# Kernel optimization log

Hardware: AMD Instinct MI355X
Metric: run time of the kernel (lower is better)

The kernel has to match this reference:

```python
import jax, jax.numpy as jnp
import numpy as np
from functools import partial

B, C, H, W = 64, 3, 64, 64
D = 64            # hidden_dim == slot dim
S = 7             # num_slots
ITERS = 3
EPS_ATTN = 1e-8
MLP_HID = 128     # max(dim, 128)


def conv5_same(x, w, b):
    # x: [B, Cin, H, W], w: [Cout, Cin, 5, 5]
    y = jax.lax.conv_general_dilated(
        x, w, window_strides=(1, 1), padding='SAME',
        dimension_numbers=('NCHW', 'OIHW', 'NCHW'))
    return y + b[None, :, None, None]


def layernorm(x, w, b, eps):
    mu = jnp.mean(x, axis=-1, keepdims=True)
    var = jnp.var(x, axis=-1, keepdims=True)
    return (x - mu) * jax.lax.rsqrt(var + eps) * w + b


def build_grid(h, w):
    rr = jnp.linspace(0.0, 1.0, h)
    cc = jnp.linspace(0.0, 1.0, w)
    g = jnp.stack(jnp.meshgrid(rr, cc, indexing='ij'), axis=-1)  # [H,W,2]
    return jnp.concatenate([g, 1.0 - g], axis=-1)                # [H,W,4]


def setup_inputs() -> dict:
    key = jax.random.key(0)
    ks = jax.random.split(key, 32)
    sc = lambda fan: 1.0 / np.sqrt(fan)
    inp = {
        'image': jax.random.normal(ks[0], (B, C, H, W), jnp.float32),
        'slots_noise': jax.random.normal(ks[1], (B, S, D), jnp.float32),
        'conv0_w': jax.random.normal(ks[2], (D, 3, 5, 5), jnp.float32) * sc(3 * 25),
        'conv0_b': jnp.zeros((D,), jnp.float32),
        'conv1_w': jax.random.normal(ks[3], (D, D, 5, 5), jnp.float32) * sc(D * 25),
        'conv1_b': jnp.zeros((D,), jnp.float32),
        'conv2_w': jax.random.normal(ks[4], (D, D, 5, 5), jnp.float32) * sc(D * 25),
        'conv2_b': jnp.zeros((D,), jnp.float32),
        'conv3_w': jax.random.normal(ks[5], (D, D, 5, 5), jnp.float32) * sc(D * 25),
        'conv3_b': jnp.zeros((D,), jnp.float32),
        'pos_w': jax.random.normal(ks[6], (D, 4), jnp.float32) * sc(4),
        'pos_b': jnp.zeros((D,), jnp.float32),
        'fc1_w': jax.random.normal(ks[7], (D, D), jnp.float32) * sc(D),
        'fc1_b': jnp.zeros((D,), jnp.float32),
        'fc2_w': jax.random.normal(ks[8], (D, D), jnp.float32) * sc(D),
        'fc2_b': jnp.zeros((D,), jnp.float32),
        'slots_mu': jax.random.uniform(ks[9], (1, 1, D), jnp.float32, -0.3, 0.3),
        'slots_log_sigma': jax.random.uniform(ks[10], (1, 1, D), jnp.float32, -0.3, 0.3),
        'q_w': jax.random.normal(ks[11], (D, D), jnp.float32) * sc(D),
        'k_w': jax.random.normal(ks[12], (D, D), jnp.float32) * sc(D),
        'v_w': jax.random.normal(ks[13], (D, D), jnp.float32) * sc(D),
        'gru_w_ih': jax.random.normal(ks[14], (3 * D, D), jnp.float32) * sc(D),
        'gru_w_hh': jax.random.normal(ks[15], (3 * D, D), jnp.float32) * sc(D),
        'gru_b_ih': jnp.zeros((3 * D,), jnp.float32),
        'gru_b_hh': jnp.zeros((3 * D,), jnp.float32),
        'mlp1_w': jax.random.normal(ks[16], (MLP_HID, D), jnp.float32) * sc(D),
        'mlp1_b': jnp.zeros((MLP_HID,), jnp.float32),
        'mlp2_w': jax.random.normal(ks[17], (D, MLP_HID), jnp.float32) * sc(MLP_HID),
        'mlp2_b': jnp.zeros((D,), jnp.float32),
        'ln_in_w': jnp.ones((D,), jnp.float32),
        'ln_in_b': jnp.zeros((D,), jnp.float32),
        'ln_slots_w': jnp.ones((D,), jnp.float32),
        'ln_slots_b': jnp.zeros((D,), jnp.float32),
        'ln_ff_w': jnp.ones((D,), jnp.float32),
        'ln_ff_b': jnp.zeros((D,), jnp.float32),
    }
    return inp


def reference(image, slots_noise, conv0_w, conv0_b, conv1_w, conv1_b,
              conv2_w, conv2_b, conv3_w, conv3_b, pos_w, pos_b,
              fc1_w, fc1_b, fc2_w, fc2_b, slots_mu, slots_log_sigma,
              q_w, k_w, v_w, gru_w_ih, gru_w_hh, gru_b_ih, gru_b_hh,
              mlp1_w, mlp1_b, mlp2_w, mlp2_b,
              ln_in_w, ln_in_b, ln_slots_w, ln_slots_b, ln_ff_w, ln_ff_b):
    b = image.shape[0]
    # --- CNN encoder ---
    x = jax.nn.relu(conv5_same(image, conv0_w, conv0_b))
    x = jax.nn.relu(conv5_same(x, conv1_w, conv1_b))
    x = jax.nn.relu(conv5_same(x, conv2_w, conv2_b))
    x = jax.nn.relu(conv5_same(x, conv3_w, conv3_b))
    x = jnp.transpose(x, (0, 2, 3, 1))                 # [B,H,W,D]
    pos = build_grid(x.shape[1], x.shape[2]) @ pos_w.T + pos_b
    x = x + pos[None]
    x = x.reshape(b, -1, D)                            # [B,N,D]
    # LayerNorm over (N, D) jointly, fresh affine (w=1, b=0), eps=1e-5
    mu = jnp.mean(x, axis=(1, 2), keepdims=True)
    var = jnp.var(x, axis=(1, 2), keepdims=True)
    x = (x - mu) * jax.lax.rsqrt(var + 1e-5)
    # --- fc MLP ---
    x = jax.nn.relu(x @ fc1_w.T + fc1_b) @ fc2_w.T + fc2_b
    # --- Slot attention ---
    scale = D ** (-0.5)
    slots = slots_mu + jnp.exp(slots_log_sigma) * slots_noise  # [B,S,D]
    inp = layernorm(x, ln_in_w, ln_in_b, 1e-3)
    k = inp @ k_w.T                                    # [B,N,D]
    v = inp @ v_w.T
    for _ in range(ITERS):
        slots_prev = slots
        q = layernorm(slots, ln_slots_w, ln_slots_b, 1e-3) @ q_w.T  # [B,S,D]
        dots = jnp.einsum('bid,bjd->bij', q, k) * scale             # [B,S,N]
        attn = jax.nn.softmax(dots, axis=1) + EPS_ATTN              # over slots
        attn = attn / jnp.sum(attn, axis=-1, keepdims=True)
        updates = jnp.einsum('bjd,bij->bid', v, attn)               # [B,S,D]
        # GRUCell(updates, slots_prev)
        gi = updates @ gru_w_ih.T + gru_b_ih                        # [B,S,3D]
        gh = slots_prev @ gru_w_hh.T + gru_b_hh
        i_r, i_z, i_n = jnp.split(gi, 3, axis=-1)
        h_r, h_z, h_n = jnp.split(gh, 3, axis=-1)
        r = jax.nn.sigmoid(i_r + h_r)
        z = jax.nn.sigmoid(i_z + h_z)
        n = jnp.tanh(i_n + r * h_n)
        slots = (1.0 - z) * n + z * slots_prev
        # residual MLP
        h = layernorm(slots, ln_ff_w, ln_ff_b, 1e-3)
        slots = slots + (jax.nn.relu(h @ mlp1_w.T + mlp1_b) @ mlp2_w.T + mlp2_b)
    return slots
```

## Files before the change

### kernel.cpp

```cpp
#include <hip/hip_runtime.h>

#define HW 64
#define BATCH 64
#define DDIM 64
#define NSLOT 7
#define NPOS 4096

typedef __attribute__((ext_vector_type(8))) short short8;
typedef __attribute__((ext_vector_type(4))) short short4v;
typedef __attribute__((ext_vector_type(4))) float floatx4;

__device__ __forceinline__ float wave_sum(float x) {
  #pragma unroll
  for (int o = 32; o >= 1; o >>= 1) x += __shfl_xor(x, o, 64);
  return x;
}

__device__ __forceinline__ unsigned short f2bf(float f) {
  unsigned int u = __float_as_uint(f);
  return (unsigned short)((u + 0x7fffu + ((u >> 16) & 1u)) >> 16);
}
__device__ __forceinline__ float bf2f(unsigned short u) {
  return __uint_as_float(((unsigned int)u) << 16);
}
__device__ __forceinline__ short4v pack4(float a, float b, float c, float d) {
  short4v s;
  s.x = (short)f2bf(a); s.y = (short)f2bf(b);
  s.z = (short)f2bf(c); s.w = (short)f2bf(d);
  return s;
}

__global__ __launch_bounds__(256) void prep_w(
    const float* __restrict__ w1, const float* __restrict__ w2,
    const float* __restrict__ w3, unsigned short* __restrict__ wp)
{
  int idx = blockIdx.x * 256 + threadIdx.x;
  if (idx >= 3 * 102400) return;
  int L = idx / 102400;
  int rem = idx - L * 102400;
  int tap = rem >> 12;
  int r2  = rem & 4095;
  int ks = r2 >> 11;
  int mt = (r2 >> 9) & 3;
  int l  = (r2 >> 3) & 63;
  int j  = r2 & 7;
  int oc  = mt * 16 + (l & 15);
  int cin = (ks * 4 + (l >> 4)) * 8 + j;
  const float* w = (L == 0) ? w1 : (L == 1) ? w2 : w3;
  wp[idx] = f2bf(w[(oc * 64 + cin) * 25 + tap]);
}

__global__ __launch_bounds__(256) void prep_fcw(
    const float* __restrict__ f1, const float* __restrict__ f2,
    const float* __restrict__ kw, const float* __restrict__ vw,
    unsigned short* __restrict__ dst)
{
  int idx = blockIdx.x * 256 + threadIdx.x;
  int mat = idx >> 12;
  int r = idx & 4095;
  int ks = r >> 11;
  int mt = (r >> 9) & 3;
  int l  = (r >> 3) & 63;
  int j  = r & 7;
  int oc = mt * 16 + (l & 15);
  int in = (ks * 4 + (l >> 4)) * 8 + j;
  const float* src = (mat == 0) ? f1 : (mat == 1) ? f2 : (mat == 2) ? kw : vw;
  dst[idx] = f2bf(src[oc * 64 + in]);
}

__global__ void prep_s1(const float* __restrict__ f1, float* __restrict__ s1)
{
  int oc = threadIdx.x;
  float s = 0.f;
  for (int k = 0; k < 64; k++) s += f1[oc * 64 + k];
  s1[oc] = s;
}

__global__ __launch_bounds__(256) void conv0_relu(
    const float* __restrict__ in, const float* __restrict__ wgt,
    const float* __restrict__ bias, unsigned short* __restrict__ out)
{
  constexpr int TH = 8, TW = 32, OCT = 16, CIN = 3;
  __shared__ __align__(16) float sIn[CIN][TH + 4][40];
  __shared__ __align__(16) float sW[CIN][25][OCT];

  const int bx = blockIdx.x;
  const int tx = bx & 1;
  const int ty = (bx >> 1) & 7;
  const int b  = bx >> 4;
  const int ocb = blockIdx.y * OCT;
  const int x0 = tx * TW, y0 = ty * TH;
  const int tid = threadIdx.x;

  const int sq  = tid & 63;
  const int ocq = tid >> 6;
  const int yy  = sq >> 3;
  const int xx4 = (sq & 7) << 2;
  const int oc0 = ocq << 2;

  float acc[4][4];
  #pragma unroll
  for (int o = 0; o < 4; o++)
    #pragma unroll
    for (int x = 0; x < 4; x++) acc[o][x] = 0.f;

  for (int idx = tid; idx < CIN * 12 * 36; idx += 256) {
    int c  = idx % 36;
    int r  = (idx / 36) % 12;
    int ci = idx / (36 * 12);
    int gy = y0 - 2 + r, gx = x0 - 2 + c;
    float v = 0.f;
    if (gy >= 0 && gy < HW && gx >= 0 && gx < HW)
      v = in[((b * CIN + ci) * HW + gy) * HW + gx];
    sIn[ci][r][c] = v;
  }
  for (int idx = tid; idx < CIN * 25 * OCT; idx += 256) {
    int oc  = idx & 15;
    int tap = (idx >> 4) % 25;
    int ci  = idx / (16 * 25);
    sW[ci][tap][oc] = wgt[((ocb + oc) * CIN + ci) * 25 + tap];
  }
  __syncthreads();

  for (int ci = 0; ci < CIN; ci++) {
    #pragma unroll
    for (int dy = 0; dy < 5; dy++) {
      const float* rp = &sIn[ci][yy + dy][xx4];
      float4 a0 = *(const float4*)rp;
      float4 a1 = *(const float4*)(rp + 4);
      float vals[8] = {a0.x, a0.y, a0.z, a0.w, a1.x, a1.y, a1.z, a1.w};
      #pragma unroll
      for (int dx = 0; dx < 5; dx++) {
        float4 wv = *(const float4*)&sW[ci][dy * 5 + dx][oc0];
        float wa[4] = {wv.x, wv.y, wv.z, wv.w};
        #pragma unroll
        for (int o = 0; o < 4; o++)
          #pragma unroll
          for (int x = 0; x < 4; x++)
            acc[o][x] += wa[o] * vals[dx + x];
      }
    }
  }

  float bb[4];
  #pragma unroll
  for (int o = 0; o < 4; o++) bb[o] = bias[ocb + oc0 + o];
  #pragma unroll
  for (int x = 0; x < 4; x++) {
    int pos = (b << 12) + (y0 + yy) * 64 + (x0 + xx4 + x);
    *(short4v*)&out[pos * 64 + ocb + oc0] =
        pack4(fmaxf(acc[0][x] + bb[0], 0.f), fmaxf(acc[1][x] + bb[1], 0.f),
              fmaxf(acc[2][x] + bb[2], 0.f), fmaxf(acc[3][x] + bb[3], 0.f));
  }
}

template<int FUSE_POS>
__global__ __launch_bounds__(256) void conv_mfma(
    const unsigned short* __restrict__ in, const unsigned short* __restrict__ wp,
    const float* __restrict__ bias, unsigned short* __restrict__ out,
    const float* __restrict__ pos_w, const float* __restrict__ pos_b,
    float* __restrict__ stats)
{
  extern __shared__ short lds[];
  short* sIn = lds;
  uint4* sWu0 = (uint4*)(lds + 25600);
  uint4* sWu1 = sWu0 + 512;

  const int tid = threadIdx.x;
  const int b   = blockIdx.x >> 4;
  const int tile = blockIdx.x & 15;
  const int y0 = (tile >> 2) * 16, x0 = (tile & 3) * 16;

  const uint4* in4 = (const uint4*)in;
  for (int idx = tid; idx < 3200; idx += 256) {
    int p = idx >> 3, c = idx & 7;
    int py = p / 20, px = p - py * 20;
    int gy = y0 - 2 + py, gx = x0 - 2 + px;
    uint4 v = {0u, 0u, 0u, 0u};
    if ((unsigned)gy < 64u && (unsigned)gx < 64u)
      v = in4[(((b << 12) + (gy << 6) + gx) << 3) + c];
    *(uint4*)&sIn[(p << 6) + ((c ^ (p & 7)) << 3)] = v;
  }
  const uint4* wg = (const uint4*)wp;
  sWu0[tid] = wg[tid];
  sWu0[256 + tid] = wg[256 + tid];
  uint4 r0 = wg[512 + tid];
  uint4 r1 = wg[512 + 256 + tid];
  __syncthreads();

  const int w  = tid >> 6;
  const int l  = tid & 63;
  const int lx = l & 15;
  const int kq = l >> 4;
  const int w4 = w * 4;

  floatx4 zero4 = {0.f, 0.f, 0.f, 0.f};
  floatx4 acc[4][4];
  #pragma unroll
  for (int yy = 0; yy < 4; yy++)
    #pragma unroll
    for (int mt = 0; mt < 4; mt++) acc[yy][mt] = zero4;

  int dy = 0, dx = 0;
  #pragma unroll 1
  for (int t = 0; t < 25; ++t) {
    uint4* cur = (t & 1) ? sWu1 : sWu0;
    if (t < 24) {
      uint4* alt = (t & 1) ? sWu0 : sWu1;
      alt[tid] = r0;
      alt[256 + tid] = r1;
    }
    if (t < 23) {
      r0 = wg[(t + 2) * 512 + tid];
      r1 = wg[(t + 2) * 512 + 256 + tid];
    }
    const int ix = lx + dx;
    #pragma unroll
    for (int ks = 0; ks < 2; ++ks) {
      const int kc = ks * 4 + kq;
      short8 Bf[4];
      #pragma unroll
      for (int yy = 0; yy < 4; ++yy) {
        int p = (w4 + yy + dy) * 20 + ix;
        Bf[yy] = *(const short8*)&sIn[(p << 6) + ((kc ^ (p & 7)) << 3)];
      }
      #pragma unroll
      for (int mt = 0; mt < 4; ++mt) {
        uint4 Af4 = cur[(ks * 4 + mt) * 64 + l];
        #pragma unroll
        for (int yy = 0; yy < 4; ++yy)
          acc[yy][mt] = __builtin_amdgcn_mfma_f32_16x16x32_bf16(
              *(const short8*)&Af4, Bf[yy], acc[yy][mt], 0, 0, 0);
      }
    }
    if (t < 24) __syncthreads();
    if (++dx == 5) { dx = 0; ++dy; }
  }

  float4 bv[4];
  #pragma unroll
  for (int mt = 0; mt < 4; ++mt) bv[mt] = *(const float4*)&bias[mt * 16 + kq * 4];

  float4 pw[4][4];  float pb[4][4];
  if (FUSE_POS) {
    #pragma unroll
    for (int mt = 0; mt < 4; ++mt)
      #pragma unroll
      for (int r = 0; r < 4; ++r) {
        int d = mt * 16 + kq * 4 + r;
        pw[mt][r] = *(const float4*)&pos_w[d * 4];
        pb[mt][r] = pos_b[d];
      }
  }

  const int x = x0 + lx;
  const float cx = x * (1.0f / 63.0f);
  float lsum = 0.f, lsq = 0.f;

  #pragma unroll
  for (int yy = 0; yy < 4; ++yy) {
    const int y = y0 + w4 + yy;
    const float ry = y * (1.0f / 63.0f);
    const int base = ((b << 12) + y * 64 + x) * 64;
    #pragma unroll
    for (int mt = 0; mt < 4; ++mt) {
      float v[4];
      #pragma unroll
      for (int r = 0; r < 4; ++r) {
        float f = fmaxf(acc[yy][mt][r] + bv[mt][r], 0.f);
        if (FUSE_POS) {
          f += ry * pw[mt][r].x + cx * pw[mt][r].y + (1.f - ry) * pw[mt][r].z +
               (1.f - cx) * pw[mt][r].w + pb[mt][r];
          lsum += f; lsq += f * f;
        }
        v[r] = f;
      }
      *(short4v*)&out[base + mt * 16 + kq * 4] = pack4(v[0], v[1], v[2], v[3]);
    }
  }

  if (FUSE_POS) {
    lsum = wave_sum(lsum);
    lsq  = wave_sum(lsq);
    if (l == 0) {
      atomicAdd(&stats[b * 2], lsum);
      atomicAdd(&stats[b * 2 + 1], lsq);
    }
  }
}

__global__ void finalize_stats(const float* __restrict__ stats, float* __restrict__ ms)
{
  int b = threadIdx.x;
  float s = stats[b * 2], q = stats[b * 2 + 1];
  float mean = s * (1.0f / 262144.f);
  float var  = q * (1.0f / 262144.f) - mean * mean;
  ms[b * 2] = mean;
  ms[b * 2 + 1] = rsqrtf(var + 1e-5f);
}

__global__ __launch_bounds__(256) void fc_mfma(
    const unsigned short* __restrict__ xb, const float* __restrict__ ms,
    const unsigned short* __restrict__ wall, const float* __restrict__ fc1_b,
    const float* __restrict__ s1, const float* __restrict__ fc2_b,
    const float* __restrict__ ln_w, const float* __restrict__ ln_b,
    unsigned short* __restrict__ kb, unsigned short* __restrict__ vT)
{
  __shared__ short sA[64 * 64];
  __shared__ uint4 sW[2048];
  const int tid = threadIdx.x;
  const int w = tid >> 6, l = tid & 63, lx = l & 15, kq = l >> 4;
  const int p0 = blockIdx.x * 64;
  const int b  = blockIdx.x >> 6;
  const int posb = (blockIdx.x & 63) * 64;
  const int w16 = w * 16;
  const float mean = ms[b * 2], rstd = ms[b * 2 + 1];
  const float rmu = rstd * mean;

  const uint4* wg = (const uint4*)wall;
  #pragma unroll
  for (int i = 0; i < 8; ++i) sW[i * 256 + tid] = wg[i * 256 + tid];

  {
    const uint4* x4 = (const uint4*)xb;
    int r0 = w16 + (l >> 3), c = l & 7;
    uint4 v0 = x4[((p0 + r0) << 3) + c];
    uint4 v1 = x4[((p0 + r0 + 8) << 3) + c];
    *(uint4*)&sA[(r0 << 6) + ((c ^ (r0 & 7)) << 3)] = v0;
    int r1 = r0 + 8;
    *(uint4*)&sA[(r1 << 6) + ((c ^ (r1 & 7)) << 3)] = v1;
  }
  __syncthreads();

  const int brow = w16 + lx;
  floatx4 zero4 = {0.f, 0.f, 0.f, 0.f};

  #define GEMM64(MATI, ACC)                                                   \
    {                                                                         \
      _Pragma("unroll")                                                       \
      for (int ks = 0; ks < 2; ++ks) {                                        \
        int ch = (ks * 4 + kq) ^ (brow & 7);                                  \
        short8 Bf = *(const short8*)&sA[(brow << 6) + (ch << 3)];             \
        _Pragma("unroll")                                                     \
        for (int mt = 0; mt < 4; ++mt) {                                      \
          uint4 Af = sW[(MATI) * 512 + (ks * 4 + mt) * 64 + l];               \
          ACC[mt] = __builtin_amdgcn_mfma_f32_16x16x32_bf16(                  \
              *(const short8*)&Af, Bf, ACC[mt], 0, 0, 0);                     \
        }                                                                     \
      }                                                                       \
    }

  #define LDSW(MT, SV)                                                        \
    {                                                                         \
      int ch = ((MT) * 2 + (kq >> 1)) ^ (brow & 7);                           \
      *(short4v*)&sA[(brow << 6) + (ch << 3) + ((kq & 1) << 2)] = (SV);       \
    }

  floatx4 a1[4] = {zero4, zero4, zero4, zero4};
  GEMM64(0, a1);
  #pragma unroll
  for (int mt = 0; mt < 4; ++mt) {
    float4 b1v = *(const float4*)&fc1_b[mt * 16 + kq * 4];
    float4 s1v = *(const float4*)&s1[mt * 16 + kq * 4];
    float v[4];
    v[0] = fmaxf(rstd * a1[mt][0] - rmu * s1v.x + b1v.x, 0.f);
    v[1] = fmaxf(rstd * a1[mt][1] - rmu * s1v.y + b1v.y, 0.f);
    v[2] = fmaxf(rstd * a1[mt][2] - rmu * s1v.z + b1v.z, 0.f);
    v[3] = fmaxf(rstd * a1[mt][3] - rmu * s1v.w + b1v.w, 0.f);
    LDSW(mt, pack4(v[0], v[1], v[2], v[3]));
  }

  floatx4 a2[4] = {zero4, zero4, zero4, zero4};
  GEMM64(1, a2);
  float y2[4][4];
  float ps = 0.f, pq = 0.f;
  #pragma unroll
  for (int mt = 0; mt < 4; ++mt) {
    float4 b2v = *(const float4*)&fc2_b[mt * 16 + kq * 4];
    float bb[4] = {b2v.x, b2v.y, b2v.z, b2v.w};
    #pragma unroll
    for (int r = 0; r < 4; ++r) {
      float y = a2[mt][r] + bb[r];
      y2[mt][r] = y;
      ps += y; pq += y * y;
    }
  }
  ps += __shfl_xor(ps, 16, 64);  ps += __shfl_xor(ps, 32, 64);
  pq += __shfl_xor(pq, 16, 64);  pq += __shfl_xor(pq, 32, 64);
  float mu2 = ps * (1.f / 64.f);
  float rs2 = rsqrtf(pq * (1.f / 64.f) - mu2 * mu2 + 1e-3f);
  #pragma unroll
  for (int mt = 0; mt < 4; ++mt) {
    float4 lwv = *(const float4*)&ln_w[mt * 16 + kq * 4];
    float4 lbv = *(const float4*)&ln_b[mt * 16 + kq * 4];
    float v[4];
    v[0] = (y2[mt][0] - mu2) * rs2 * lwv.x + lbv.x;
    v[1] = (y2[mt][1] - mu2) * rs2 * lwv.y + lbv.y;
    v[2] = (y2[mt][2] - mu2) * rs2 * lwv.z + lbv.z;
    v[3] = (y2[mt][3] - mu2) * rs2 * lwv.w + lbv.w;
    LDSW(mt, pack4(v[0], v[1], v[2], v[3]));
  }

  floatx4 a3[4] = {zero4, zero4, zero4, zero4};
  GEMM64(2, a3);
  const int gbase = ((p0 + brow) << 6) + kq * 4;
  #pragma unroll
  for (int mt = 0; mt < 4; ++mt)
    *(short4v*)&kb[gbase + mt * 16] = pack4(a3[mt][0], a3[mt][1], a3[mt][2], a3[mt][3]);

  floatx4 a4[4] = {zero4, zero4, zero4, zero4};
  GEMM64(3, a4);
  #pragma unroll
  for (int mt = 0; mt < 4; ++mt)
    #pragma unroll
    for (int r = 0; r < 4; ++r)
      vT[((b << 6) + mt * 16 + kq * 4 + r) * 4096 + posb + brow] = f2bf(a4[mt][r]);

  #undef GEMM64
  #undef LDSW
}

__global__ __launch_bounds__(256) void slots_init(
    const float* __restrict__ mu, const float* __restrict__ ls,
    const float* __restrict__ noise, float* __restrict__ slots)
{
  int idx = blockIdx.x * 256 + threadIdx.x;
  if (idx < BATCH * NSLOT * DDIM) {
    int d = idx & 63;
    slots[idx] = mu[d] + expf(ls[d]) * noise[idx];
  }
}

__global__ __launch_bounds__(64) void compute_q(
    const float* __restrict__ slots, const float* __restrict__ lnw,
    const float* __restrict__ lnb, const float* __restrict__ q_w,
    float* __restrict__ qout, float* __restrict__ U, float* __restrict__ T)
{
  __shared__ float sLn[64];
  const int bs = blockIdx.x;
  const int l = threadIdx.x;
  U[bs * 64 + l] = 0.f;
  if (l == 0) T[bs] = 0.f;
  float v = slots[bs * 64 + l];
  float m = wave_sum(v) * (1.f / 64.f);
  float dv = v - m;
  float var = wave_sum(dv * dv) * (1.f / 64.f);
  sLn[l] = dv * rsqrtf(var + 1e-3f) * lnw[l] + lnb[l];
  __syncthreads();
  float acc = 0.f;
  #pragma unroll
  for (int e = 0; e < 64; e += 4) {
    float4 w4 = *(const float4*)&q_w[l * 64 + e];
    acc += w4.x * sLn[e] + w4.y * sLn[e + 1] + w4.z * sLn[e + 2] + w4.w * sLn[e + 3];
  }
  qout[bs * 64 + l] = acc;
}

__global__ __launch_bounds__(256) void attn_fused(
    const unsigned short* __restrict__ kb, const float* __restrict__ q,
    const unsigned short* __restrict__ vT,
    float* __restrict__ U, float* __restrict__ T)
{
  __shared__ short sQ[16 * 64];
  __shared__ short sP[4][16 * 72];
  __shared__ float sUr[4][7 * 64];
  const int b  = blockIdx.x >> 4;
  const int jt = blockIdx.x & 15;
  const int tid = threadIdx.x;
  const int w = tid >> 6, l = tid & 63, lx = l & 15, kq = l >> 4;
  floatx4 zero4 = {0.f, 0.f, 0.f, 0.f};

  for (int i = tid; i < 1024; i += 256) {
    int s = i >> 6, d = i & 63;
    sQ[i] = (s < 7) ? (short)f2bf(q[(b * 7 + s) * 64 + d]) : (short)0;
  }
  __syncthreads();

  uint4 qA[2];
  #pragma unroll
  for (int ks = 0; ks < 2; ++ks)
    qA[ks] = *(const uint4*)&sQ[lx * 64 + (ks * 4 + kq) * 8];

  const uint4* kb4 = (const uint4*)kb;
  const int row0 = kq * 4;
  const int j0 = jt * 256 + w * 64;
  float tacc[4] = {0.f, 0.f, 0.f, 0.f};
  short* sPw = sP[w];

  #pragma unroll
  for (int jh = 0; jh < 4; ++jh) {
    const int j = j0 + jh * 16 + lx;
    floatx4 d4 = zero4;
    #pragma unroll
    for (int ks = 0; ks < 2; ++ks) {
      uint4 kB = kb4[(((b << 12) + j) << 3) + ks * 4 + kq];
      d4 = __builtin_amdgcn_mfma_f32_16x16x32_bf16(
          *(const short8*)&qA[ks], *(const short8*)&kB, d4, 0, 0, 0);
    }
    float e[4];
    float mx = -1e30f;
    #pragma unroll
    for (int r = 0; r < 4; ++r) {
      e[r] = (row0 + r < 7) ? d4[r] * 0.125f : -1e30f;
      mx = fmaxf(mx, e[r]);
    }
    mx = fmaxf(mx, __shfl_xor(mx, 16, 64));
    mx = fmaxf(mx, __shfl_xor(mx, 32, 64));
    float sum = 0.f;
    #pragma unroll
    for (int r = 0; r < 4; ++r) {
      e[r] = (row0 + r < 7) ? __expf(e[r] - mx) : 0.f;
      sum += e[r];
    }
    sum += __shfl_xor(sum, 16, 64);
    sum += __shfl_xor(sum, 32, 64);
    float inv = 1.f / sum;
    #pragma unroll
    for (int r = 0; r < 4; ++r) {
      float p = (row0 + r < 7) ? e[r] * inv + 1e-8f : 0.f;
      tacc[r] += p;
      sPw[(row0 + r) * 72 + jh * 16 + lx] = (short)f2bf(p);
    }
  }

  #pragma unroll
  for (int r = 0; r < 4; ++r) {
    if (row0 + r < 7) {
      float t = tacc[r];
      t += __shfl_xor(t, 1, 64);  t += __shfl_xor(t, 2, 64);
      t += __shfl_xor(t, 4, 64);  t += __shfl_xor(t, 8, 64);
      if (lx == 0) atomicAdd(&T[b * 7 + row0 + r], t);
    }
  }
  __syncthreads();

  floatx4 uacc[4] = {zero4, zero4, zero4, zero4};
  #pragma unroll
  for (int nt = 0; nt < 4; ++nt) {
    #pragma unroll
    for (int ks = 0; ks < 2; ++ks) {
      short8 pa = *(const short8*)&sPw[lx * 72 + ks * 32 + kq * 8];
      uint4 vB = *(const uint4*)&vT[((b << 6) + nt * 16 + lx) * 4096 +
                                    j0 + ks * 32 + kq * 8];
      uacc[nt] = __builtin_amdgcn_mfma_f32_16x16x32_bf16(
          pa, *(const short8*)&vB, uacc[nt], 0, 0, 0);
    }
  }

  #pragma unroll
  for (int nt = 0; nt < 4; ++nt)
    #pragma unroll
    for (int r = 0; r < 4; ++r)
      if (row0 + r < 7)
        sUr[w][(row0 + r) * 64 + nt * 16 + lx] = uacc[nt][r];
  __syncthreads();

  for (int i = tid; i < 448; i += 256) {
    float u = sUr[0][i] + sUr[1][i] + sUr[2][i] + sUr[3][i];
    atomicAdd(&U[b * 448 + i], u);
  }
}

__global__ __launch_bounds__(192) void gru_mlp(
    const float* __restrict__ U, const float* __restrict__ T,
    const float* __restrict__ w_ih, const float* __restrict__ w_hh,
    const float* __restrict__ b_ih, const float* __restrict__ b_hh,
    const float* __restrict__ lnfw, const float* __restrict__ lnfb,
    const float* __restrict__ m1w, const float* __restrict__ m1b,
    const float* __restrict__ m2w, const float* __restrict__ m2b,
    float* __restrict__ slots)
{
  __shared__ float sU[64], sSp[64], sGi[192], sGh[192], sH[64], sLn[64], sHid[128];
  const int bs = blockIdx.x;
  const int t = threadIdx.x;

  if (t < 64) {
    sU[t] = U[bs * 64 + t] / T[bs];
    sSp[t] = slots[bs * 64 + t];
  }
  __syncthreads();
  {
    float gi = b_ih[t], gh = b_hh[t];
    #pragma unroll
    for (int d = 0; d < 64; d += 4) {
      float4 wi = *(const float4*)&w_ih[t * 64 + d];
      float4 wh = *(const float4*)&w_hh[t * 64 + d];
      gi += wi.x * sU[d] + wi.y * sU[d + 1] + wi.z * sU[d + 2] + wi.w * sU[d + 3];
      gh += wh.x * sSp[d] + wh.y * sSp[d + 1] + wh.z * sSp[d + 2] + wh.w * sSp[d + 3];
    }
    sGi[t] = gi; sGh[t] = gh;
  }
  __syncthreads();
  if (t < 64) {
    float r = 1.f / (1.f + expf(-(sGi[t] + sGh[t])));
    float z = 1.f / (1.f + expf(-(sGi[64 + t] + sGh[64 + t])));
    float n = tanhf(sGi[128 + t] + r * sGh[128 + t]);
    float h = (1.f - z) * n + z * sSp[t];
    sH[t] = h;
    float m = wave_sum(h) * (1.f / 64.f);
    float dv = h - m;
    float var = wave_sum(dv * dv) * (1.f / 64.f);
    sLn[t] = dv * rsqrtf(var + 1e-3f) * lnfw[t] + lnfb[t];
  }
  __syncthreads();
  if (t < 128) {
    float a = m1b[t];
    #pragma unroll
    for (int d = 0; d < 64; d += 4) {
      float4 w = *(const float4*)&m1w[t * 64 + d];
      a += w.x * sLn[d] + w.y * sLn[d + 1] + w.z * sLn[d + 2] + w.w * sLn[d + 3];
    }
    sHid[t] = fmaxf(a, 0.f);
  }
  __syncthreads();
  if (t < 64) {
    float a = m2b[t];
    #pragma unroll
    for (int k = 0; k < 128; k += 4) {
      float4 w = *(const float4*)&m2w[t * 128 + k];
      a += w.x * sHid[k] + w.y * sHid[k + 1] + w.z * sHid[k + 2] + w.w * sHid[k + 3];
    }
    slots[bs * 64 + t] = sH[t] + a;
  }
}

extern "C" void kernel_launch(void* const* d_in, const int* in_sizes, int n_in,
                              void* d_out, int out_size, void* d_ws, size_t ws_size,
                              hipStream_t stream)
{
  const float* image    = (const float*)d_in[0];
  const float* noise    = (const float*)d_in[1];
  const float* conv0_w  = (const float*)d_in[2];
  const float* conv0_b  = (const float*)d_in[3];
  const float* conv1_w  = (const float*)d_in[4];
  const float* conv1_b  = (const float*)d_in[5];
  const float* conv2_w  = (const float*)d_in[6];
  const float* conv2_b  = (const float*)d_in[7];
  const float* conv3_w  = (const float*)d_in[8];
  const float* conv3_b  = (const float*)d_in[9];
  const float* pos_w    = (const float*)d_in[10];
  const float* pos_b    = (const float*)d_in[11];
  const float* fc1_w    = (const float*)d_in[12];
  const float* fc1_b    = (const float*)d_in[13];
  const float* fc2_w    = (const float*)d_in[14];
  const float* fc2_b    = (const float*)d_in[15];
  const float* slots_mu = (const float*)d_in[16];
  const float* slots_ls = (const float*)d_in[17];
  const float* q_w      = (const float*)d_in[18];
  const float* k_w      = (const float*)d_in[19];
  const float* v_w      = (const float*)d_in[20];
  const float* gru_w_ih = (const float*)d_in[21];
  const float* gru_w_hh = (const float*)d_in[22];
  const float* gru_b_ih = (const float*)d_in[23];
  const float* gru_b_hh = (const float*)d_in[24];
  const float* mlp1_w   = (const float*)d_in[25];
  const float* mlp1_b   = (const float*)d_in[26];
  const float* mlp2_w   = (const float*)d_in[27];
  const float* mlp2_b   = (const float*)d_in[28];
  const float* ln_in_w  = (const float*)d_in[29];
  const float* ln_in_b  = (const float*)d_in[30];
  const float* ln_sl_w  = (const float*)d_in[31];
  const float* ln_sl_b  = (const float*)d_in[32];
  const float* ln_ff_w  = (const float*)d_in[33];
  const float* ln_ff_b  = (const float*)d_in[34];

  float* ws = (float*)d_ws;
  float* R1   = ws;
  float* R2   = R1 + 16777216;
  float* Pbuf = R2 + 16777216;
  float* qbuf  = Pbuf + 1835008;
  float* slots = qbuf + 28672;
  float* Ubuf  = slots + 28672;
  float* Tbuf  = Ubuf + 28672;
  float* stats = Tbuf + 448;
  float* ms    = stats + 128;

  unsigned short* Wp  = (unsigned short*)Pbuf;
  unsigned short* wfc = Wp + 307200;
  float* s1f = (float*)(wfc + 16384);
  unsigned short* Y0 = (unsigned short*)R1;
  unsigned short* Y1 = (unsigned short*)R2;
  unsigned short* xb = (unsigned short*)R2;
  unsigned short* kb = (unsigned short*)R1;
  unsigned short* vT = kb + 16777216;

  prep_w<<<1200, 256, 0, stream>>>(conv1_w, conv2_w, conv3_w, Wp);
  prep_fcw<<<64, 256, 0, stream>>>(fc1_w, fc2_w, k_w, v_w, wfc);
  prep_s1<<<1, 64, 0, stream>>>(fc1_w, s1f);
  hipMemsetAsync(stats, 0, 128 * sizeof(float), stream);

  dim3 cgrid(1024, 4);
  conv0_relu<<<cgrid, 256, 0, stream>>>(image, conv0_w, conv0_b, Y0);
  conv_mfma<0><<<1024, 256, 67584, stream>>>(Y0, Wp,          conv1_b, Y1,
                                             nullptr, nullptr, nullptr);
  conv_mfma<0><<<1024, 256, 67584, stream>>>(Y1, Wp + 102400, conv2_b, Y0,
                                             nullptr, nullptr, nullptr);
  conv_mfma<1><<<1024, 256, 67584, stream>>>(Y0, Wp + 204800, conv3_b, xb,
                                             pos_w, pos_b, stats);
  finalize_stats<<<1, 64, 0, stream>>>(stats, ms);

  fc_mfma<<<4096, 256, 0, stream>>>(xb, ms, wfc, fc1_b, s1f, fc2_b,
                                    ln_in_w, ln_in_b, kb, vT);

  slots_init<<<112, 256, 0, stream>>>(slots_mu, slots_ls, noise, slots);

  for (int it = 0; it < 3; it++) {
    compute_q<<<448, 64, 0, stream>>>(slots, ln_sl_w, ln_sl_b, q_w, qbuf,
                                      Ubuf, Tbuf);
    attn_fused<<<1024, 256, 0, stream>>>(kb, qbuf, vT, Ubuf, Tbuf);
    gru_mlp<<<448, 192, 0, stream>>>(Ubuf, Tbuf, gru_w_ih, gru_w_hh, gru_b_ih,
                                     gru_b_hh, ln_ff_w, ln_ff_b, mlp1_w, mlp1_b,
                                     mlp2_w, mlp2_b, slots);
  }

  hipMemcpyAsync(d_out, slots, 28672 * sizeof(float), hipMemcpyDeviceToDevice, stream);
}
```

Measured before the change: 555.9 us.

## Load conv input tiles directly from global memory instead of staging in LDS

Drops the 20x20x64 bf16 input halo tile that each conv_mfma block staged in shared memory. Each MFMA B-fragment is now read straight from global memory per filter tap, with zero-padding decided by a bounds check. Only the double-buffered weight tile stays in LDS, and launch bounds ask for 4 blocks per CU to raise occupancy. In exchange, every input element is re-read from global memory up to 25 times (once per tap), so the kernel now depends on L1/L2 hit rates. The dependent global loads also sit inside the MFMA loop with no explicit prefetch.

```diff
diff --git a/kernel.cpp b/kernel.cpp
--- a/kernel.cpp
+++ b/kernel.cpp
@@ -155,16 +155,13 @@
 }
 
 template<int FUSE_POS>
-__global__ __launch_bounds__(256) void conv_mfma(
+__global__ __launch_bounds__(256, 4) void conv_mfma(
     const unsigned short* __restrict__ in, const unsigned short* __restrict__ wp,
     const float* __restrict__ bias, unsigned short* __restrict__ out,
     const float* __restrict__ pos_w, const float* __restrict__ pos_b,
     float* __restrict__ stats)
 {
-  extern __shared__ short lds[];
-  short* sIn = lds;
-  uint4* sWu0 = (uint4*)(lds + 25600);
-  uint4* sWu1 = sWu0 + 512;
+  __shared__ uint4 sWu[2][512];
 
   const int tid = threadIdx.x;
   const int b   = blockIdx.x >> 4;
@@ -172,18 +169,9 @@
   const int y0 = (tile >> 2) * 16, x0 = (tile & 3) * 16;
 
   const uint4* in4 = (const uint4*)in;
-  for (int idx = tid; idx < 3200; idx += 256) {
-    int p = idx >> 3, c = idx & 7;
-    int py = p / 20, px = p - py * 20;
-    int gy = y0 - 2 + py, gx = x0 - 2 + px;
-    uint4 v = {0u, 0u, 0u, 0u};
-    if ((unsigned)gy < 64u && (unsigned)gx < 64u)
-      v = in4[(((b << 12) + (gy << 6) + gx) << 3) + c];
-    *(uint4*)&sIn[(p << 6) + ((c ^ (p & 7)) << 3)] = v;
-  }
   const uint4* wg = (const uint4*)wp;
-  sWu0[tid] = wg[tid];
-  sWu0[256 + tid] = wg[256 + tid];
+  sWu[0][tid] = wg[tid];
+  sWu[0][256 + tid] = wg[256 + tid];
   uint4 r0 = wg[512 + tid];
   uint4 r1 = wg[512 + 256 + tid];
   __syncthreads();
@@ -201,12 +189,14 @@
     #pragma unroll
     for (int mt = 0; mt < 4; mt++) acc[yy][mt] = zero4;
 
+  const int gxl = x0 - 2 + lx;
+
   int dy = 0, dx = 0;
   #pragma unroll 1
   for (int t = 0; t < 25; ++t) {
-    uint4* cur = (t & 1) ? sWu1 : sWu0;
+    uint4* cur = sWu[t & 1];
     if (t < 24) {
-      uint4* alt = (t & 1) ? sWu0 : sWu1;
+      uint4* alt = sWu[(t + 1) & 1];
       alt[tid] = r0;
       alt[256 + tid] = r1;
     }
@@ -214,23 +204,31 @@
       r0 = wg[(t + 2) * 512 + tid];
       r1 = wg[(t + 2) * 512 + 256 + tid];
     }
-    const int ix = lx + dx;
+    const int gx = gxl + dx;
+    const bool xok = ((unsigned)gx < 64u);
+    uint4 Braw[4][2];
+    #pragma unroll
+    for (int yy = 0; yy < 4; ++yy) {
+      const int gy = y0 + w4 + yy + dy - 2;
+      const bool ok = xok && ((unsigned)gy < 64u);
+      const int pbase = (((b << 12) + (gy << 6) + gx) << 3);
+      #pragma unroll
+      for (int ks = 0; ks < 2; ++ks) {
+        uint4 v = {0u, 0u, 0u, 0u};
+        if (ok) v = in4[pbase + ks * 4 + kq];
+        Braw[yy][ks] = v;
+      }
+    }
     #pragma unroll
     for (int ks = 0; ks < 2; ++ks) {
-      const int kc = ks * 4 + kq;
-      short8 Bf[4];
-      #pragma unroll
-      for (int yy = 0; yy < 4; ++yy) {
-        int p = (w4 + yy + dy) * 20 + ix;
-        Bf[yy] = *(const short8*)&sIn[(p << 6) + ((kc ^ (p & 7)) << 3)];
-      }
       #pragma unroll
       for (int mt = 0; mt < 4; ++mt) {
         uint4 Af4 = cur[(ks * 4 + mt) * 64 + l];
         #pragma unroll
         for (int yy = 0; yy < 4; ++yy)
           acc[yy][mt] = __builtin_amdgcn_mfma_f32_16x16x32_bf16(
-              *(const short8*)&Af4, Bf[yy], acc[yy][mt], 0, 0, 0);
+              *(const short8*)&Af4, *(const short8*)&Braw[yy][ks],
+              acc[yy][mt], 0, 0, 0);
       }
     }
     if (t < 24) __syncthreads();
@@ -691,12 +689,12 @@
 
   dim3 cgrid(1024, 4);
   conv0_relu<<<cgrid, 256, 0, stream>>>(image, conv0_w, conv0_b, Y0);
-  conv_mfma<0><<<1024, 256, 67584, stream>>>(Y0, Wp,          conv1_b, Y1,
-                                             nullptr, nullptr, nullptr);
-  conv_mfma<0><<<1024, 256, 67584, stream>>>(Y1, Wp + 102400, conv2_b, Y0,
-                                             nullptr, nullptr, nullptr);
-  conv_mfma<1><<<1024, 256, 67584, stream>>>(Y0, Wp + 204800, conv3_b, xb,
-                                             pos_w, pos_b, stats);
+  conv_mfma<0><<<1024, 256, 0, stream>>>(Y0, Wp,          conv1_b, Y1,
+                                         nullptr, nullptr, nullptr);
+  conv_mfma<0><<<1024, 256, 0, stream>>>(Y1, Wp + 102400, conv2_b, Y0,
+                                         nullptr, nullptr, nullptr);
+  conv_mfma<1><<<1024, 256, 0, stream>>>(Y0, Wp + 204800, conv3_b, xb,
+                                         pos_w, pos_b, stats);
   finalize_stats<<<1, 64, 0, stream>>>(stats, ms);
 
   fc_mfma<<<4096, 256, 0, stream>>>(xb, ms, wfc, fc1_b, s1f, fc2_b,
```

Result: slower. 717.2 us (+29.0%).

## Fuse q projection into attention kernel and replace atomics with partial-sum slabs

Applied to the files above, without the earlier changes.

The separate compute_q kernel is removed; each attention block now recomputes the slot layernorm and q projection for its batch in shared memory. Global atomicAdd accumulation of U and T is replaced by per-block partial slabs that gru_mlp sums over 16 tiles. This drops three kernel launches and the atomics, at the cost of redundant q computation in 16 blocks per batch. The layernorm output is also rounded to bf16 before the projection, which slightly changes precision.

```diff
diff --git a/kernel.cpp b/kernel.cpp
--- a/kernel.cpp
+++ b/kernel.cpp
@@ -431,48 +431,41 @@
   }
 }
 
-__global__ __launch_bounds__(64) void compute_q(
+__global__ __launch_bounds__(256) void attn_fused(
     const float* __restrict__ slots, const float* __restrict__ lnw,
     const float* __restrict__ lnb, const float* __restrict__ q_w,
-    float* __restrict__ qout, float* __restrict__ U, float* __restrict__ T)
-{
-  __shared__ float sLn[64];
-  const int bs = blockIdx.x;
-  const int l = threadIdx.x;
-  U[bs * 64 + l] = 0.f;
-  if (l == 0) T[bs] = 0.f;
-  float v = slots[bs * 64 + l];
-  float m = wave_sum(v) * (1.f / 64.f);
-  float dv = v - m;
-  float var = wave_sum(dv * dv) * (1.f / 64.f);
-  sLn[l] = dv * rsqrtf(var + 1e-3f) * lnw[l] + lnb[l];
-  __syncthreads();
-  float acc = 0.f;
-  #pragma unroll
-  for (int e = 0; e < 64; e += 4) {
-    float4 w4 = *(const float4*)&q_w[l * 64 + e];
-    acc += w4.x * sLn[e] + w4.y * sLn[e + 1] + w4.z * sLn[e + 2] + w4.w * sLn[e + 3];
-  }
-  qout[bs * 64 + l] = acc;
-}
-
-__global__ __launch_bounds__(256) void attn_fused(
-    const unsigned short* __restrict__ kb, const float* __restrict__ q,
-    const unsigned short* __restrict__ vT,
-    float* __restrict__ U, float* __restrict__ T)
-{
+    const unsigned short* __restrict__ kb, const unsigned short* __restrict__ vT,
+    float* __restrict__ Upart, float* __restrict__ Tpart)
+{
+  __shared__ short sLN[7 * 64];
   __shared__ short sQ[16 * 64];
   __shared__ short sP[4][16 * 72];
   __shared__ float sUr[4][7 * 64];
+  __shared__ float sT[4][8];
   const int b  = blockIdx.x >> 4;
   const int jt = blockIdx.x & 15;
   const int tid = threadIdx.x;
   const int w = tid >> 6, l = tid & 63, lx = l & 15, kq = l >> 4;
   floatx4 zero4 = {0.f, 0.f, 0.f, 0.f};
 
-  for (int i = tid; i < 1024; i += 256) {
-    int s = i >> 6, d = i & 63;
-    sQ[i] = (s < 7) ? (short)f2bf(q[(b * 7 + s) * 64 + d]) : (short)0;
+  for (int i = tid; i < 1024; i += 256) sQ[i] = 0;
+
+  for (int s = w; s < 7; s += 4) {
+    float v = slots[(b * 7 + s) * 64 + l];
+    float m = wave_sum(v) * (1.f / 64.f);
+    float dv = v - m;
+    float var = wave_sum(dv * dv) * (1.f / 64.f);
+    sLN[s * 64 + l] = (short)f2bf(dv * rsqrtf(var + 1e-3f) * lnw[l] + lnb[l]);
+  }
+  for (int s = w; s < 7; s += 4) {
+    float acc = 0.f;
+    #pragma unroll
+    for (int e = 0; e < 64; e += 4) {
+      float4 w4v = *(const float4*)&q_w[l * 64 + e];
+      acc += w4v.x * bf2f(sLN[s * 64 + e])     + w4v.y * bf2f(sLN[s * 64 + e + 1])
+           + w4v.z * bf2f(sLN[s * 64 + e + 2]) + w4v.w * bf2f(sLN[s * 64 + e + 3]);
+    }
+    sQ[s * 64 + l] = (short)f2bf(acc);
   }
   __syncthreads();
 
@@ -529,7 +522,7 @@
       float t = tacc[r];
       t += __shfl_xor(t, 1, 64);  t += __shfl_xor(t, 2, 64);
       t += __shfl_xor(t, 4, 64);  t += __shfl_xor(t, 8, 64);
-      if (lx == 0) atomicAdd(&T[b * 7 + row0 + r], t);
+      if (lx == 0) sT[w][row0 + r] = t;
     }
   }
   __syncthreads();
@@ -555,14 +548,15 @@
         sUr[w][(row0 + r) * 64 + nt * 16 + lx] = uacc[nt][r];
   __syncthreads();
 
-  for (int i = tid; i < 448; i += 256) {
-    float u = sUr[0][i] + sUr[1][i] + sUr[2][i] + sUr[3][i];
-    atomicAdd(&U[b * 448 + i], u);
-  }
+  const int slab = b * 16 + jt;
+  for (int i = tid; i < 448; i += 256)
+    Upart[slab * 448 + i] = sUr[0][i] + sUr[1][i] + sUr[2][i] + sUr[3][i];
+  if (tid < 7)
+    Tpart[slab * 7 + tid] = sT[0][tid] + sT[1][tid] + sT[2][tid] + sT[3][tid];
 }
 
 __global__ __launch_bounds__(192) void gru_mlp(
-    const float* __restrict__ U, const float* __restrict__ T,
+    const float* __restrict__ Upart, const float* __restrict__ Tpart,
     const float* __restrict__ w_ih, const float* __restrict__ w_hh,
     const float* __restrict__ b_ih, const float* __restrict__ b_hh,
     const float* __restrict__ lnfw, const float* __restrict__ lnfb,
@@ -572,10 +566,17 @@
 {
   __shared__ float sU[64], sSp[64], sGi[192], sGh[192], sH[64], sLn[64], sHid[128];
   const int bs = blockIdx.x;
+  const int b = bs / 7, s = bs - b * 7;
   const int t = threadIdx.x;
 
   if (t < 64) {
-    sU[t] = U[bs * 64 + t] / T[bs];
+    float u = 0.f, Ts = 0.f;
+    #pragma unroll 4
+    for (int jt = 0; jt < 16; ++jt) {
+      u  += Upart[(b * 16 + jt) * 448 + s * 64 + t];
+      Ts += Tpart[(b * 16 + jt) * 7 + s];
+    }
+    sU[t] = u / Ts;
     sSp[t] = slots[bs * 64 + t];
   }
   __syncthreads();
@@ -678,6 +679,8 @@
   unsigned short* Wp  = (unsigned short*)Pbuf;
   unsigned short* wfc = Wp + 307200;
   float* s1f = (float*)(wfc + 16384);
+  float* Upart = Pbuf + 262144;
+  float* Tpart = Upart + 458752;
   unsigned short* Y0 = (unsigned short*)R1;
   unsigned short* Y1 = (unsigned short*)R2;
   unsigned short* xb = (unsigned short*)R2;
@@ -705,12 +708,11 @@
   slots_init<<<112, 256, 0, stream>>>(slots_mu, slots_ls, noise, slots);
 
   for (int it = 0; it < 3; it++) {
-    compute_q<<<448, 64, 0, stream>>>(slots, ln_sl_w, ln_sl_b, q_w, qbuf,
-                                      Ubuf, Tbuf);
-    attn_fused<<<1024, 256, 0, stream>>>(kb, qbuf, vT, Ubuf, Tbuf);
-    gru_mlp<<<448, 192, 0, stream>>>(Ubuf, Tbuf, gru_w_ih, gru_w_hh, gru_b_ih,
-                                     gru_b_hh, ln_ff_w, ln_ff_b, mlp1_w, mlp1_b,
-                                     mlp2_w, mlp2_b, slots);
+    attn_fused<<<1024, 256, 0, stream>>>(slots, ln_sl_w, ln_sl_b, q_w,
+                                         kb, vT, Upart, Tpart);
+    gru_mlp<<<448, 192, 0, stream>>>(Upart, Tpart, gru_w_ih, gru_w_hh,
+                                     gru_b_ih, gru_b_hh, ln_ff_w, ln_ff_b,
+                                     mlp1_w, mlp1_b, mlp2_w, mlp2_b, slots);
   }
 
   hipMemcpyAsync(d_out, slots, 28672 * sizeof(float), hipMemcpyDeviceToDevice, stream);
```

After: 499.1 us (median of 2 runs). 1.11x faster.
